# Performance work log

Measured on AMD Instinct MI355X. Metric: run time of the kernel, lower is better.

## Reference

```python
import jax, jax.numpy as jnp
import numpy as np

H = 2048   # hidden_size
NH = 32    # n_head
HS = 64    # head_size
B, T = 2, 4096
D_DECAY, D_AAA, D_MV, D_GATE = 96, 96, 64, 256


def setup_inputs() -> dict:
    key = jax.random.key(0)
    ks = jax.random.split(key, 30)
    rn = lambda k, s, sc=0.02: jax.random.normal(k, s, jnp.float32) * sc
    d = {}
    d['x'] = jax.random.normal(ks[0], (B, T, H), jnp.float32)
    d['shift_state_in'] = jax.random.normal(ks[1], (B, H), jnp.float32)
    d['wkv_state_in'] = jnp.zeros((B, NH, HS, HS), jnp.float32)
    d['v_first_val'] = jax.random.normal(ks[2], (B, T, H), jnp.float32)
    for i, n in enumerate(['x_r', 'x_w', 'x_k', 'x_v', 'x_a', 'x_g']):
        d[n] = jax.random.uniform(ks[3 + i], (H,), jnp.float32)
    d['w0'] = rn(ks[9], (H,)) - 4.0
    d['w1'] = rn(ks[10], (H, D_DECAY)); d['w2'] = rn(ks[11], (D_DECAY, H))
    d['a0'] = rn(ks[12], (H,)); d['a1'] = rn(ks[13], (H, D_AAA)); d['a2'] = rn(ks[14], (D_AAA, H))
    d['v0'] = rn(ks[15], (H,)) + 1.0; d['v1'] = rn(ks[16], (H, D_MV)); d['v2'] = rn(ks[17], (D_MV, H))
    d['g1'] = rn(ks[18], (H, D_GATE)); d['g2'] = rn(ks[19], (D_GATE, H))
    d['k_k'] = jnp.full((H,), 0.85, jnp.float32)
    d['k_a'] = jnp.ones((H,), jnp.float32)
    d['r_k'] = rn(ks[20], (NH, HS))
    s = 1.0 / np.sqrt(H)
    d['W_r'] = jax.random.normal(ks[21], (H, H), jnp.float32) * s
    d['W_k'] = jax.random.normal(ks[22], (H, H), jnp.float32) * s
    d['W_v'] = jax.random.normal(ks[23], (H, H), jnp.float32) * s
    d['W_o'] = jax.random.normal(ks[24], (H, H), jnp.float32) * s
    d['ln_w'] = jnp.ones((H,), jnp.float32)
    d['ln_b'] = jnp.zeros((H,), jnp.float32)
    return d


def _forward(x, shift_state_in, wkv_state_in, v_first_val, x_r, x_w, x_k, x_v, x_a, x_g,
             w0, w1, w2, a0, a1, a2, v0, v1, v2, g1, g2, k_k, k_a, r_k,
             W_r, W_k, W_v, W_o, ln_w, ln_b):
    Bx, Tx, C = x.shape
    # token shift: previous token embedding (shift_state for t=0)
    xprev = jnp.concatenate([shift_state_in[:, None, :], x[:, :-1]], axis=1)
    dx = xprev - x
    xr, xw, xk, xv, xa, xg = (x + dx * m for m in (x_r, x_w, x_k, x_v, x_a, x_g))
    r = xr @ W_r.T
    k = xk @ W_k.T
    v = xv @ W_v.T
    # soft-clamped log-decay (<= -0.5)
    w_raw = -jax.nn.softplus(-(w0 + jnp.tanh(xw @ w1) @ w2)) - 0.5
    # layer_id > 0: residual mix with first-layer value
    v = v + (v_first_val - v) * jax.nn.sigmoid(v0 + (xv @ v1) @ v2)
    a = jax.nn.sigmoid(a0 + (xa @ a1) @ a2)          # in-context learning rate
    g = jax.nn.sigmoid(xg @ g1) @ g2                 # output gate
    kk = (k * k_k).reshape(Bx, Tx, NH, HS)
    kk = kk / jnp.maximum(jnp.linalg.norm(kk, axis=-1, keepdims=True), 1e-12)  # F.normalize
    kk = kk.reshape(Bx, Tx, C)
    k = k * (1.0 + (a - 1.0) * k_a)
    w = jnp.exp(-jnp.exp(w_raw))                     # per-channel decay in (0,1)
    heads = lambda t: t.reshape(Bx, Tx, NH, HS).transpose(1, 0, 2, 3)  # [T,B,NH,HS]
    rs, ws, ks_, vs, kks, as_ = map(heads, (r, w, k, v, kk, a))

    def step(S, inp):
        # S: [B,NH,HS(value),HS(key)]
        rt, wt, kt, vt, kkt, at = inp
        sa = jnp.einsum('bhvk,bhk->bhv', S, -kkt)
        S = (S * wt[:, :, None, :]
             + sa[:, :, :, None] * (kkt * at)[:, :, None, :]
             + vt[:, :, :, None] * kt[:, :, None, :])
        return S, jnp.einsum('bhvk,bhk->bhv', S, rt)

    wkv_state_out, y = jax.lax.scan(step, wkv_state_in, (rs, ws, ks_, vs, kks, as_))
    y = y.transpose(1, 0, 2, 3)                      # [B,T,NH,HS]
    # GroupNorm(n_head groups, eps=1e-5*head_size)
    mu = y.mean(-1, keepdims=True)
    var = y.var(-1, keepdims=True)
    y = ((y - mu) / jnp.sqrt(var + 1e-5 * HS)).reshape(Bx, Tx, C) * ln_w + ln_b
    rk = (r.reshape(Bx, Tx, NH, HS) * k.reshape(Bx, Tx, NH, HS) * r_k).sum(-1, keepdims=True)
    y = y + (rk * v.reshape(Bx, Tx, NH, HS)).reshape(Bx, Tx, C)
    out = (y * g) @ W_o.T
    return out, x[:, -1], wkv_state_out, v_first_val


def reference(x, shift_state_in, wkv_state_in, v_first_val, x_r, x_w, x_k, x_v, x_a, x_g,
              w0, w1, w2, a0, a1, a2, v0, v1, v2, g1, g2, k_k, k_a, r_k,
              W_r, W_k, W_v, W_o, ln_w, ln_b):
    return _forward(x, shift_state_in, wkv_state_in, v_first_val, x_r, x_w, x_k, x_v, x_a, x_g,
                    w0, w1, w2, a0, a1, a2, v0, v1, v2, g1, g2, k_k, k_a, r_k,
                    W_r, W_k, W_v, W_o, ln_w, ln_b)
```

## Files before the change

### kernel.cpp

```cpp
#include <hip/hip_runtime.h>

typedef unsigned short u16;
typedef __attribute__((ext_vector_type(4))) float f32x4;
typedef __attribute__((ext_vector_type(8))) __bf16 bf16x8;
typedef __attribute__((ext_vector_type(8))) unsigned short u16x8;
typedef __attribute__((ext_vector_type(4))) unsigned short u16x4;

#define DI static __device__ __forceinline__

DI float bfu2f(u16 u){ unsigned int x = ((unsigned int)u)<<16; float f; __builtin_memcpy(&f,&x,4); return f; }
DI u16 f2bfu(float f){ __bf16 h = (__bf16)f; u16 u; __builtin_memcpy(&u,&h,2); return u; }
DI float sigm(float x){ return 1.f/(1.f+expf(-x)); }

DI void gload_lds16(const void* g, void* l) {
  __builtin_amdgcn_global_load_lds(
      (const __attribute__((address_space(1))) unsigned int*)g,
      (__attribute__((address_space(3))) unsigned int*)l, 16, 0, 0);
}

template<bool OBF16>
__global__ __launch_bounds__(256) void gemm128_k(
    const u16* __restrict__ A, const u16* __restrict__ Bt,
    void* __restrict__ Cp, int M, int N, int K)
{
  __shared__ alignas(16) u16 As[128*64];
  __shared__ alignas(16) u16 Bs[128*64];
  const int tid = threadIdx.x;
  const int wid = tid >> 6, lane = tid & 63;
  const int wm = wid >> 1, wn = wid & 1;
  const int l15 = lane & 15, q = lane >> 4;
  const int m0 = blockIdx.x * 128, n0 = blockIdx.y * 128;
  const int sr = (wid << 3) + (lane >> 3);
  const int sc = (lane & 7) << 3;
  f32x4 acc[4][4];
  #pragma unroll
  for (int i=0;i<4;i++)
    #pragma unroll
    for (int j=0;j<4;j++) acc[i][j] = f32x4{0.f,0.f,0.f,0.f};

  char* la = (char*)As + (size_t)wid*1024;
  char* lb = (char*)Bs + (size_t)wid*1024;
  for (int k0 = 0; k0 < K; k0 += 64) {
    const u16* ga = A  + (size_t)(m0 + sr)*K + k0 + sc;
    const u16* gb = Bt + (size_t)(n0 + sr)*K + k0 + sc;
    #pragma unroll
    for (int it = 0; it < 4; ++it) {
      gload_lds16(ga + (size_t)(32*it)*K, la + it*4096);
      gload_lds16(gb + (size_t)(32*it)*K, lb + it*4096);
    }
    __syncthreads();
    #pragma unroll
    for (int ks = 0; ks < 64; ks += 32) {
      bf16x8 af[4], bfv[4];
      #pragma unroll
      for (int i=0;i<4;i++) af[i]  = *(const bf16x8*)&As[(wm*64 + i*16 + l15)*64 + ks + q*8];
      #pragma unroll
      for (int j=0;j<4;j++) bfv[j] = *(const bf16x8*)&Bs[(wn*64 + j*16 + l15)*64 + ks + q*8];
      #pragma unroll
      for (int i=0;i<4;i++)
        #pragma unroll
        for (int j=0;j<4;j++)
          acc[i][j] = __builtin_amdgcn_mfma_f32_16x16x32_bf16(af[i], bfv[j], acc[i][j], 0, 0, 0);
    }
    __syncthreads();
  }
  #pragma unroll
  for (int i=0;i<4;i++)
    #pragma unroll
    for (int j=0;j<4;j++)
      #pragma unroll
      for (int rr=0;rr<4;rr++) {
        const int gm = m0 + wm*64 + i*16 + q*4 + rr;
        const int gn = n0 + wn*64 + j*16 + l15;
        const size_t o = (size_t)gm * (size_t)N + gn;
        if constexpr (OBF16) ((u16*)Cp)[o] = f2bfu(acc[i][j][rr]);
        else                 ((float*)Cp)[o] = acc[i][j][rr];
      }
}

constexpr int LDW = 72;

template<bool MIX, bool WNK, bool ABF16, bool OBF16, int EPI=0>
__global__ __launch_bounds__(256) void gemm_k(
    const void* __restrict__ Ap, const float* __restrict__ dxp, const float* __restrict__ mixp,
    const float* __restrict__ Wp, void* __restrict__ Cp, int M, int N, int K)
{
  __shared__ alignas(16) __bf16 As[64*LDW];
  __shared__ alignas(16) __bf16 Bs[64*LDW];
  const int tid = threadIdx.x;
  const int m0 = blockIdx.x * 64;
  const int n0 = blockIdx.y * 64;
  const int lane = tid & 63, wid = tid >> 6;
  const int wm = wid >> 1, wn = wid & 1;
  const int l15 = lane & 15, q = lane >> 4;
  f32x4 acc[2][2] = {{{0.f,0.f,0.f,0.f},{0.f,0.f,0.f,0.f}},
                     {{0.f,0.f,0.f,0.f},{0.f,0.f,0.f,0.f}}};

  for (int k0 = 0; k0 < K; k0 += 64) {
    {
      const int kc = (tid & 7) * 8;
      const int r0 = tid >> 3;
      #pragma unroll
      for (int it = 0; it < 2; ++it) {
        const int row = r0 + 32*it;
        const size_t gmK = (size_t)(m0 + row) * (size_t)K;
        const int gk = k0 + kc;
        if constexpr (ABF16) {
          const u16* A16 = (const u16*)Ap;
          u16x8 u;
          if (gk + 7 < K) u = *(const u16x8*)(A16 + gmK + gk);
          else {
            #pragma unroll
            for (int e=0;e<8;e++) u[e] = (gk+e < K) ? A16[gmK + gk + e] : (u16)0;
          }
          *(u16x8*)&As[row*LDW + kc] = u;
        } else {
          const float* A32 = (const float*)Ap;
          float f[8];
          if (gk + 7 < K) {
            f32x4 va = *(const f32x4*)(A32 + gmK + gk);
            f32x4 vb = *(const f32x4*)(A32 + gmK + gk + 4);
            if constexpr (MIX) {
              f32x4 d0 = *(const f32x4*)(dxp + gmK + gk);
              f32x4 d1 = *(const f32x4*)(dxp + gmK + gk + 4);
              f32x4 c0 = *(const f32x4*)(mixp + gk);
              f32x4 c1 = *(const f32x4*)(mixp + gk + 4);
              va = va + d0*c0; vb = vb + d1*c1;
            }
            #pragma unroll
            for (int e=0;e<4;e++){ f[e]=va[e]; f[4+e]=vb[e]; }
          } else {
            #pragma unroll
            for (int e=0;e<8;e++){
              const int kk2 = gk+e;
              float xv = 0.f;
              if (kk2 < K) {
                xv = A32[gmK + kk2];
                if constexpr (MIX) xv = fmaf(dxp[gmK+kk2], mixp[kk2], xv);
              }
              f[e] = xv;
            }
          }
          bf16x8 v8;
          #pragma unroll
          for (int e=0;e<8;e++) v8[e] = (__bf16)f[e];
          *(bf16x8*)&As[row*LDW + kc] = v8;
        }
      }
    }
    if constexpr (WNK) {
      const int kc = (tid & 7) * 8;
      const int r0 = tid >> 3;
      #pragma unroll
      for (int it = 0; it < 2; ++it) {
        const int row = r0 + 32*it;
        const int gn = n0 + row;
        const int gk = k0 + kc;
        float f[8];
        if (gn < N && gk + 7 < K) {
          const size_t o = (size_t)gn * (size_t)K + gk;
          f32x4 va = *(const f32x4*)(Wp + o);
          f32x4 vb = *(const f32x4*)(Wp + o + 4);
          #pragma unroll
          for (int e=0;e<4;e++){ f[e]=va[e]; f[4+e]=vb[e]; }
        } else {
          #pragma unroll
          for (int e=0;e<8;e++) f[e] = (gn < N && gk+e < K) ? Wp[(size_t)gn*K + gk + e] : 0.f;
        }
        bf16x8 v8;
        #pragma unroll
        for (int e=0;e<8;e++) v8[e] = (__bf16)f[e];
        *(bf16x8*)&Bs[row*LDW + kc] = v8;
      }
    } else {
      const int nc = (tid & 15) * 4;
      const int kr = tid >> 4;
      #pragma unroll
      for (int it = 0; it < 4; ++it) {
        const int kk = kr + 16*it;
        const int gk = k0 + kk;
        f32x4 v = {0.f,0.f,0.f,0.f};
        if (gk < K) {
          const int gn = n0 + nc;
          if (gn + 3 < N) v = *(const f32x4*)(Wp + (size_t)gk*N + gn);
          else {
            #pragma unroll
            for (int e=0;e<4;e++) if (gn+e < N) v[e] = Wp[(size_t)gk*N + gn + e];
          }
        }
        #pragma unroll
        for (int e=0;e<4;e++) Bs[(nc+e)*LDW + kk] = (__bf16)v[e];
      }
    }
    __syncthreads();
    #pragma unroll
    for (int ks = 0; ks < 64; ks += 32) {
      bf16x8 af[2], bfv[2];
      #pragma unroll
      for (int i=0;i<2;i++) af[i]  = *(const bf16x8*)&As[(wm*32 + i*16 + l15)*LDW + ks + q*8];
      #pragma unroll
      for (int i=0;i<2;i++) bfv[i] = *(const bf16x8*)&Bs[(wn*32 + i*16 + l15)*LDW + ks + q*8];
      #pragma unroll
      for (int i=0;i<2;i++)
        #pragma unroll
        for (int j=0;j<2;j++)
          acc[i][j] = __builtin_amdgcn_mfma_f32_16x16x32_bf16(af[i], bfv[j], acc[i][j], 0, 0, 0);
    }
    __syncthreads();
  }
  #pragma unroll
  for (int i=0;i<2;i++) {
    #pragma unroll
    for (int j=0;j<2;j++) {
      #pragma unroll
      for (int rr=0;rr<4;rr++) {
        const int gm = m0 + wm*32 + i*16 + q*4 + rr;
        const int gn = n0 + wn*32 + j*16 + l15;
        if (gn < N) {
          const size_t o = (size_t)gm * (size_t)N + gn;
          if constexpr (EPI == 1) {
            float* C = (float*)Cp;
            const float s = sigm(mixp[gn] + acc[i][j][rr]);
            const float vG = C[o];
            C[o] = vG + (dxp[o] - vG) * s;
          } else if constexpr (OBF16) {
            ((u16*)Cp)[o] = f2bfu(acc[i][j][rr]);
          } else {
            ((float*)Cp)[o] = acc[i][j][rr];
          }
        }
      }
    }
  }
}

__global__ void mix_cast_k(const float* __restrict__ x, const float* __restrict__ shift,
    const float* __restrict__ mr, const float* __restrict__ mw, const float* __restrict__ mk,
    const float* __restrict__ mv, const float* __restrict__ ma, const float* __restrict__ mg,
    u16* __restrict__ xr_b, u16* __restrict__ xw_b, u16* __restrict__ xk_b,
    u16* __restrict__ xv_b, u16* __restrict__ xa_b, u16* __restrict__ xg_b,
    float* __restrict__ xlast, int T_, int B_)
{
  const int Hh = 2048;
  size_t e4 = (size_t)blockIdx.x*blockDim.x + threadIdx.x;
  size_t total4 = (size_t)B_*T_*Hh/4;
  if (e4 >= total4) return;
  size_t e = e4*4;
  size_t th = (size_t)T_*Hh;
  size_t b = e / th; size_t rem = e - b*th;
  int t = (int)(rem / Hh); int c = (int)(rem & (Hh-1));
  f32x4 xv4 = *(const f32x4*)(x+e);
  f32x4 xp = t ? *(const f32x4*)(x+e-Hh) : *(const f32x4*)(shift + b*Hh + c);
  f32x4 dx = xp - xv4;
  if (t == T_-1) *(f32x4*)(xlast + b*Hh + c) = xv4;
  #define EMIT(mp, dst) { \
    f32x4 mc = *(const f32x4*)(mp + c); \
    f32x4 r_ = xv4 + dx*mc; \
    u16x4 o_; \
    o_[0]=f2bfu(r_[0]); o_[1]=f2bfu(r_[1]); o_[2]=f2bfu(r_[2]); o_[3]=f2bfu(r_[3]); \
    *(u16x4*)(dst + e) = o_; }
  EMIT(mr, xr_b) EMIT(mw, xw_b) EMIT(mk, xk_b)
  EMIT(mv, xv_b) EMIT(ma, xa_b) EMIT(mg, xg_b)
  #undef EMIT
}

__global__ void castw_k(const float* __restrict__ src, u16* __restrict__ dst, long n4){
  long i = (long)blockIdx.x*blockDim.x + threadIdx.x;
  if (i < n4) {
    f32x4 v = ((const f32x4*)src)[i];
    u16x4 o; o[0]=f2bfu(v[0]); o[1]=f2bfu(v[1]); o[2]=f2bfu(v[2]); o[3]=f2bfu(v[3]);
    ((u16x4*)dst)[i] = o;
  }
}

__global__ void ew_tanh_k(u16* p, long n){
  long i = (long)blockIdx.x*blockDim.x + threadIdx.x;
  if (i < n) p[i] = f2bfu(tanhf(bfu2f(p[i])));
}
__global__ void ew_sig_k(u16* p, long n){
  long i = (long)blockIdx.x*blockDim.x + threadIdx.x;
  if (i < n) p[i] = f2bfu(sigm(bfu2f(p[i])));
}
__global__ void ew_w_k(float* p, const float* __restrict__ w0, long n){
  long i = (long)blockIdx.x*blockDim.x + threadIdx.x;
  if (i < n) {
    int c = (int)(i & 2047);
    float z = -(w0[c] + p[i]);
    float sp = (z > 20.f) ? z : log1pf(expf(z));
    p[i] = expf(-expf(-sp - 0.5f));
  }
}
__global__ void ew_a_k(u16* p, const float* __restrict__ a0, long n){
  long i = (long)blockIdx.x*blockDim.x + threadIdx.x;
  if (i < n) { int c = (int)(i & 2047); p[i] = f2bfu(sigm(a0[c] + bfu2f(p[i]))); }
}
__global__ void copy4_k(float* __restrict__ dst, const float* __restrict__ src, long n4){
  long i = (long)blockIdx.x*blockDim.x + threadIdx.x;
  if (i < n4) ((f32x4*)dst)[i] = ((const f32x4*)src)[i];
}

__global__ __launch_bounds__(64) __attribute__((amdgpu_waves_per_eu(1, 4)))
void scan_k(
    const u16* __restrict__ rb, const float* __restrict__ wb, const u16* __restrict__ kb,
    const float* __restrict__ vb, const u16* __restrict__ ab,
    const float* __restrict__ kkw, const float* __restrict__ kaw,
    const float* __restrict__ S0, float* __restrict__ yb, float* __restrict__ Sout, int T_)
{
  const int Hh = 2048, NHl = 32;
  const int blk = blockIdx.x;
  const int b = blk >> 5, h = blk & 31;
  const int lane = threadIdx.x;
  float S[64];
  const size_t sbase = (((size_t)b*NHl + h)*64 + lane)*64;
  #pragma unroll
  for (int i=0;i<64;i++) S[i] = S0[sbase+i];
  const float kkc = kkw[h*64+lane], kac = kaw[h*64+lane];
  __shared__ alignas(16) float lw[64], lkk[64], lka[64], lke[64], lr[64];
  size_t idx = (size_t)b*T_*Hh + (size_t)h*64 + lane;
  float rv = bfu2f(rb[idx]), wv = wb[idx], kv = bfu2f(kb[idx]), vv = vb[idx], av = bfu2f(ab[idx]);
  for (int t=0; t<T_; ++t) {
    float kk = kv * kkc;
    float ssum = kk*kk;
    #pragma unroll
    for (int m=1;m<64;m<<=1) ssum += __shfl_xor(ssum, m, 64);
    float inv = 1.f / fmaxf(sqrtf(ssum), 1e-12f);
    float kkn = kk * inv;
    float ke  = kv * (1.f + (av - 1.f)*kac);
    lw[lane]=wv; lkk[lane]=kkn; lka[lane]=kkn*av; lke[lane]=ke; lr[lane]=rv;
    const float vt = vv;
    __syncthreads();
    float nrv=0.f,nwv=0.f,nkv=0.f,nvv=0.f,nav=0.f;
    if (t+1 < T_) {
      const size_t ni = idx + Hh;
      nrv = bfu2f(rb[ni]); nwv = wb[ni]; nkv = bfu2f(kb[ni]); nvv = vb[ni]; nav = bfu2f(ab[ni]);
    }
    const f32x4* KK4 = (const f32x4*)lkk;
    const f32x4* W4  = (const f32x4*)lw;
    const f32x4* KA4 = (const f32x4*)lka;
    const f32x4* KE4 = (const f32x4*)lke;
    const f32x4* R4  = (const f32x4*)lr;
    float sa0=0.f,sa1=0.f,sa2=0.f,sa3=0.f;
    #pragma unroll
    for (int qq=0;qq<16;qq++){
      f32x4 k4 = KK4[qq];
      sa0 = fmaf(S[4*qq+0], k4[0], sa0);
      sa1 = fmaf(S[4*qq+1], k4[1], sa1);
      sa2 = fmaf(S[4*qq+2], k4[2], sa2);
      sa3 = fmaf(S[4*qq+3], k4[3], sa3);
    }
    const float sa = -((sa0+sa1)+(sa2+sa3));
    float y0=0.f,y1=0.f,y2=0.f,y3=0.f;
    #pragma unroll
    for (int qq=0;qq<16;qq++){
      f32x4 w4=W4[qq], a4=KA4[qq], e4=KE4[qq], r4=R4[qq];
      float s_;
      s_ = fmaf(vt, e4[0], fmaf(sa, a4[0], S[4*qq+0]*w4[0])); S[4*qq+0]=s_; y0 = fmaf(s_, r4[0], y0);
      s_ = fmaf(vt, e4[1], fmaf(sa, a4[1], S[4*qq+1]*w4[1])); S[4*qq+1]=s_; y1 = fmaf(s_, r4[1], y1);
      s_ = fmaf(vt, e4[2], fmaf(sa, a4[2], S[4*qq+2]*w4[2])); S[4*qq+2]=s_; y2 = fmaf(s_, r4[2], y2);
      s_ = fmaf(vt, e4[3], fmaf(sa, a4[3], S[4*qq+3]*w4[3])); S[4*qq+3]=s_; y3 = fmaf(s_, r4[3], y3);
    }
    yb[idx] = (y0+y1)+(y2+y3);
    __syncthreads();
    rv=nrv; wv=nwv; kv=nkv; vv=nvv; av=nav;
    idx += Hh;
  }
  #pragma unroll
  for (int i=0;i<64;i++) Sout[sbase+i] = S[i];
}

__global__ __launch_bounds__(128) __attribute__((amdgpu_waves_per_eu(1, 4)))
void chunk_mu_k(
    const float* __restrict__ wb, const u16* __restrict__ kb,
    const float* __restrict__ vb, const u16* __restrict__ ab,
    const float* __restrict__ kkw, const float* __restrict__ kaw,
    float* __restrict__ Mbuf, float* __restrict__ Ubuf, int T_, int NC)
{
  const int Hh = 2048;
  const int ch = blockIdx.x;
  const int c  = ch % NC;
  const int bh = ch / NC;
  const int b = bh >> 5, h = bh & 31;
  const int lane = threadIdx.x & 63;
  const int wvv  = threadIdx.x >> 6;

  float S[64];
  const bool idrow = (wvv == 0);
  #pragma unroll
  for (int i=0;i<64;i++) S[i] = (idrow && lane == i) ? 1.f : 0.f;

  const int hc = h*64 + lane;
  const float kkc = kkw[hc], kac = kaw[hc];

  __shared__ alignas(16) float LA[2][4][64];
  float* Lw  = LA[wvv][0];
  float* Lkk = LA[wvv][1];
  float* Lka = LA[wvv][2];
  float* Lke = LA[wvv][3];

  size_t idx = ((size_t)b*T_ + (size_t)c*64)*Hh + h*64 + lane;
  float kv = bfu2f(kb[idx]), wv_ = wb[idx], av = bfu2f(ab[idx]), vv = vb[idx];

  for (int j=0; j<64; ++j) {
    float kk = kv * kkc;
    float ssum = kk*kk;
    #pragma unroll
    for (int m=1;m<64;m<<=1) ssum += __shfl_xor(ssum, m, 64);
    float inv = 1.f / fmaxf(sqrtf(ssum), 1e-12f);
    float kkn = kk * inv;
    Lw[lane]=wv_; Lkk[lane]=kkn; Lka[lane]=kkn*av; Lke[lane]=kv*(1.f+(av-1.f)*kac);
    const float vtv = vv;
    __syncthreads();
    float nk=0.f,nw=0.f,na=0.f,nv=0.f;
    if (j+1 < 64) {
      const size_t ni = idx + Hh;
      nk = bfu2f(kb[ni]); nw = wb[ni]; na = bfu2f(ab[ni]); nv = vb[ni];
    }
    const f32x4* KK4 = (const f32x4*)Lkk;
    const f32x4* W4  = (const f32x4*)Lw;
    const f32x4* KA4 = (const f32x4*)Lka;
    const f32x4* KE4 = (const f32x4*)Lke;
    float sa0=0.f,sa1=0.f,sa2=0.f,sa3=0.f;
    #pragma unroll
    for (int qq=0;qq<16;qq++){
      f32x4 k4 = KK4[qq];
      sa0 = fmaf(S[4*qq+0], k4[0], sa0);
      sa1 = fmaf(S[4*qq+1], k4[1], sa1);
      sa2 = fmaf(S[4*qq+2], k4[2], sa2);
      sa3 = fmaf(S[4*qq+3], k4[3], sa3);
    }
    const float sa = -((sa0+sa1)+(sa2+sa3));
    if (idrow) {
      #pragma unroll
      for (int qq=0;qq<16;qq++){
        f32x4 w4=W4[qq], a4=KA4[qq];
        S[4*qq+0] = fmaf(sa, a4[0], S[4*qq+0]*w4[0]);
        S[4*qq+1] = fmaf(sa, a4[1], S[4*qq+1]*w4[1]);
        S[4*qq+2] = fmaf(sa, a4[2], S[4*qq+2]*w4[2]);
        S[4*qq+3] = fmaf(sa, a4[3], S[4*qq+3]*w4[3]);
      }
    } else {
      #pragma unroll
      for (int qq=0;qq<16;qq++){
        f32x4 w4=W4[qq], a4=KA4[qq], e4=KE4[qq];
        S[4*qq+0] = fmaf(vtv, e4[0], fmaf(sa, a4[0], S[4*qq+0]*w4[0]));
        S[4*qq+1] = fmaf(vtv, e4[1], fmaf(sa, a4[1], S[4*qq+1]*w4[1]));
        S[4*qq+2] = fmaf(vtv, e4[2], fmaf(sa, a4[2], S[4*qq+2]*w4[2]));
        S[4*qq+3] = fmaf(vtv, e4[3], fmaf(sa, a4[3], S[4*qq+3]*w4[3]));
      }
    }
    __syncthreads();
    kv=nk; wv_=nw; av=na; vv=nv;
    idx += Hh;
  }
  float* dst = (idrow ? Mbuf : Ubuf) + (size_t)ch*4096 + (size_t)lane*64;
  #pragma unroll
  for (int qq=0;qq<16;qq++)
    *(f32x4*)(dst + 4*qq) = f32x4{S[4*qq+0],S[4*qq+1],S[4*qq+2],S[4*qq+3]};
}

__global__ __launch_bounds__(256) void propagate_k(
    const float* __restrict__ Mbuf, const float* __restrict__ Ubuf,
    const float* __restrict__ S0, float* __restrict__ SSbuf, float* __restrict__ Sout, int NC)
{
  const int bh   = blockIdx.x >> 2;
  const int v0r  = (blockIdx.x & 3) * 16;
  const int tid  = threadIdx.x;
  const int lane = tid & 63;
  const int wvv  = tid >> 6;

  __shared__ float MT[64*65];
  __shared__ float Srow[16][64];

  #pragma unroll
  for (int i=0;i<4;i++) {
    const int v = v0r + wvv*4 + i;
    Srow[wvv*4+i][lane] = S0[((size_t)bh*64 + v)*64 + lane];
  }

  const size_t mbase = (size_t)bh * NC * 4096;
  f32x4 mreg[4];
  #pragma unroll
  for (int it=0; it<4; ++it)
    mreg[it] = *(const f32x4*)(Mbuf + mbase + it*1024 + tid*4);

  for (int c=0; c<NC; ++c) {
    const size_t chB = mbase + (size_t)c*4096;
    #pragma unroll
    for (int it=0; it<4; ++it) {
      const int base = it*1024 + tid*4;
      const int j = base >> 6;
      const int k = base & 63;
      #pragma unroll
      for (int e=0;e<4;e++) MT[(k+e)*65 + j] = mreg[it][e];
    }
    __syncthreads();
    if (c+1 < NC) {
      #pragma unroll
      for (int it=0; it<4; ++it)
        mreg[it] = *(const f32x4*)(Mbuf + chB + 4096 + it*1024 + tid*4);
    }
    #pragma unroll
    for (int i=0;i<4;i++)
      SSbuf[chB + (size_t)(v0r + wvv*4 + i)*64 + lane] = Srow[wvv*4+i][lane];
    float u[4];
    #pragma unroll
    for (int i=0;i<4;i++)
      u[i] = Ubuf[chB + (size_t)(v0r + wvv*4 + i)*64 + lane];
    float acc[4] = {0.f,0.f,0.f,0.f};
    #pragma unroll
    for (int j4=0; j4<16; ++j4) {
      float m0_ = MT[lane*65 + j4*4 + 0];
      float m1_ = MT[lane*65 + j4*4 + 1];
      float m2_ = MT[lane*65 + j4*4 + 2];
      float m3_ = MT[lane*65 + j4*4 + 3];
      #pragma unroll
      for (int i=0;i<4;i++) {
        f32x4 s4 = *(const f32x4*)&Srow[wvv*4+i][j4*4];
        acc[i] = fmaf(s4[0], m0_, acc[i]);
        acc[i] = fmaf(s4[1], m1_, acc[i]);
        acc[i] = fmaf(s4[2], m2_, acc[i]);
        acc[i] = fmaf(s4[3], m3_, acc[i]);
      }
    }
    #pragma unroll
    for (int i=0;i<4;i++) Srow[wvv*4+i][lane] = acc[i] + u[i];
    __syncthreads();
  }
  #pragma unroll
  for (int i=0;i<4;i++) {
    const int v = v0r + wvv*4 + i;
    Sout[((size_t)bh*64 + v)*64 + lane] = Srow[wvv*4+i][lane];
  }
}

__global__ __launch_bounds__(64) __attribute__((amdgpu_waves_per_eu(1, 4)))
void replay_k(
    const u16* __restrict__ rb, const float* __restrict__ wb, const u16* __restrict__ kb,
    const float* __restrict__ vb, const u16* __restrict__ ab,
    const float* __restrict__ kkw, const float* __restrict__ kaw,
    const float* __restrict__ SSbuf, float* __restrict__ yb, int T_, int NC)
{
  const int Hh = 2048;
  const int ch = blockIdx.x;
  const int c  = ch % NC;
  const int bh = ch / NC;
  const int b = bh >> 5, h = bh & 31;
  const int lane = threadIdx.x;
  float S[64];
  const float* sp = SSbuf + (size_t)ch*4096 + (size_t)lane*64;
  #pragma unroll
  for (int qq=0;qq<16;qq++){
    f32x4 v4 = *(const f32x4*)(sp + 4*qq);
    S[4*qq+0]=v4[0]; S[4*qq+1]=v4[1]; S[4*qq+2]=v4[2]; S[4*qq+3]=v4[3];
  }
  const float kkc = kkw[h*64+lane], kac = kaw[h*64+lane];
  __shared__ alignas(16) float lw[64], lkk[64], lka[64], lke[64], lr[64];
  size_t idx = ((size_t)b*T_ + (size_t)c*64)*Hh + (size_t)h*64 + lane;
  float rv = bfu2f(rb[idx]), wv = wb[idx], kv = bfu2f(kb[idx]), vv = vb[idx], av = bfu2f(ab[idx]);
  for (int t=0; t<64; ++t) {
    float kk = kv * kkc;
    float ssum = kk*kk;
    #pragma unroll
    for (int m=1;m<64;m<<=1) ssum += __shfl_xor(ssum, m, 64);
    float inv = 1.f / fmaxf(sqrtf(ssum), 1e-12f);
    float kkn = kk * inv;
    float ke  = kv * (1.f + (av - 1.f)*kac);
    lw[lane]=wv; lkk[lane]=kkn; lka[lane]=kkn*av; lke[lane]=ke; lr[lane]=rv;
    const float vt = vv;
    __syncthreads();
    float nrv=0.f,nwv=0.f,nkv=0.f,nvv=0.f,nav=0.f;
    if (t+1 < 64) {
      const size_t ni = idx + Hh;
      nrv = bfu2f(rb[ni]); nwv = wb[ni]; nkv = bfu2f(kb[ni]); nvv = vb[ni]; nav = bfu2f(ab[ni]);
    }
    const f32x4* KK4 = (const f32x4*)lkk;
    const f32x4* W4  = (const f32x4*)lw;
    const f32x4* KA4 = (const f32x4*)lka;
    const f32x4* KE4 = (const f32x4*)lke;
    const f32x4* R4  = (const f32x4*)lr;
    float sa0=0.f,sa1=0.f,sa2=0.f,sa3=0.f;
    #pragma unroll
    for (int qq=0;qq<16;qq++){
      f32x4 k4 = KK4[qq];
      sa0 = fmaf(S[4*qq+0], k4[0], sa0);
      sa1 = fmaf(S[4*qq+1], k4[1], sa1);
      sa2 = fmaf(S[4*qq+2], k4[2], sa2);
      sa3 = fmaf(S[4*qq+3], k4[3], sa3);
    }
    const float sa = -((sa0+sa1)+(sa2+sa3));
    float y0=0.f,y1=0.f,y2=0.f,y3=0.f;
    #pragma unroll
    for (int qq=0;qq<16;qq++){
      f32x4 w4=W4[qq], a4=KA4[qq], e4=KE4[qq], r4=R4[qq];
      float s_;
      s_ = fmaf(vt, e4[0], fmaf(sa, a4[0], S[4*qq+0]*w4[0])); S[4*qq+0]=s_; y0 = fmaf(s_, r4[0], y0);
      s_ = fmaf(vt, e4[1], fmaf(sa, a4[1], S[4*qq+1]*w4[1])); S[4*qq+1]=s_; y1 = fmaf(s_, r4[1], y1);
      s_ = fmaf(vt, e4[2], fmaf(sa, a4[2], S[4*qq+2]*w4[2])); S[4*qq+2]=s_; y2 = fmaf(s_, r4[2], y2);
      s_ = fmaf(vt, e4[3], fmaf(sa, a4[3], S[4*qq+3]*w4[3])); S[4*qq+3]=s_; y3 = fmaf(s_, r4[3], y3);
    }
    yb[idx] = (y0+y1)+(y2+y3);
    __syncthreads();
    rv=nrv; wv=nwv; kv=nkv; vv=nvv; av=nav;
    idx += Hh;
  }
}

__global__ __launch_bounds__(256) void post_k(
    const float* __restrict__ yb, const u16* __restrict__ rb, const u16* __restrict__ kb,
    const u16* __restrict__ ab, const u16* __restrict__ gb, const float* __restrict__ vb,
    const float* __restrict__ kaw, const float* __restrict__ rkw,
    const float* __restrict__ lnw, const float* __restrict__ lnb, u16* __restrict__ zb)
{
  const int wid = threadIdx.x >> 6, lane = threadIdx.x & 63;
  const size_t unit = (size_t)blockIdx.x*4 + wid;
  const size_t bt = unit >> 5; const int h = (int)(unit & 31);
  const size_t idx = bt*2048 + (size_t)h*64 + lane;
  const int hc = h*64 + lane;
  const float yv = yb[idx];
  const float rv = bfu2f(rb[idx]), kv = bfu2f(kb[idx]), av = bfu2f(ab[idx]);
  const float ke = kv*(1.f + (av-1.f)*kaw[hc]);
  float s1 = yv, s2 = yv*yv, rk = rv*ke*rkw[hc];
  #pragma unroll
  for (int m=1;m<64;m<<=1){
    s1 += __shfl_xor(s1,m,64);
    s2 += __shfl_xor(s2,m,64);
    rk += __shfl_xor(rk,m,64);
  }
  const float mean = s1 * (1.f/64.f);
  const float var  = s2 * (1.f/64.f) - mean*mean;
  const float rstd = rsqrtf(var + 6.4e-4f);
  const float zn = (yv-mean)*rstd*lnw[hc] + lnb[hc] + rk*vb[idx];
  zb[idx] = f2bfu(zn * bfu2f(gb[idx]));
}

extern "C" void kernel_launch(void* const* d_in, const int* in_sizes, int n_in,
                              void* d_out, int out_size, void* d_ws, size_t ws_size,
                              hipStream_t stream)
{
  const float* x      = (const float*)d_in[0];
  const float* shift  = (const float*)d_in[1];
  const float* wkv0   = (const float*)d_in[2];
  const float* vfirst = (const float*)d_in[3];
  const float* xr = (const float*)d_in[4];
  const float* xw = (const float*)d_in[5];
  const float* xk = (const float*)d_in[6];
  const float* xv = (const float*)d_in[7];
  const float* xa = (const float*)d_in[8];
  const float* xg = (const float*)d_in[9];
  const float* w0 = (const float*)d_in[10];
  const float* w1 = (const float*)d_in[11];
  const float* w2 = (const float*)d_in[12];
  const float* a0 = (const float*)d_in[13];
  const float* a1 = (const float*)d_in[14];
  const float* a2 = (const float*)d_in[15];
  const float* v0 = (const float*)d_in[16];
  const float* v1 = (const float*)d_in[17];
  const float* v2 = (const float*)d_in[18];
  const float* g1 = (const float*)d_in[19];
  const float* g2 = (const float*)d_in[20];
  const float* k_k = (const float*)d_in[21];
  const float* k_a = (const float*)d_in[22];
  const float* r_k = (const float*)d_in[23];
  const float* W_r = (const float*)d_in[24];
  const float* W_k = (const float*)d_in[25];
  const float* W_v = (const float*)d_in[26];
  const float* W_o = (const float*)d_in[27];
  const float* ln_w = (const float*)d_in[28];
  const float* ln_b = (const float*)d_in[29];

  const int H = 2048, NH = 32;
  const int BH = in_sizes[1];
  const int B  = BH / H;
  const long BTH = (long)in_sizes[0];
  const int T  = (int)(BTH / BH);
  const int M  = (int)(BTH / H);

  float* out0 = (float*)d_out;
  float* out1 = out0 + BTH;
  float* out2 = out1 + BH;
  float* out3 = out2 + (size_t)B*NH*64*64;

  char* ws = (char*)d_ws;
  u16* mixb = (u16*)ws;  ws += (size_t)BTH*12;
  u16* xr_b = mixb + 0*BTH;
  u16* xw_b = mixb + 1*BTH;
  u16* xk_b = mixb + 2*BTH;
  u16* xv_b = mixb + 3*BTH;
  u16* xa_b = mixb + 4*BTH;
  u16* xg_b = mixb + 5*BTH;
  float* Mbuf  = (float*)mixb;
  float* Ubuf  = Mbuf + BTH;
  float* SSbuf = Ubuf + BTH;
  u16*   zb16  = (u16*)mixb;
  u16* rb   = (u16*)ws;  ws += BTH*2;
  u16* kb   = (u16*)ws;  ws += BTH*2;
  u16* ab   = (u16*)ws;  ws += BTH*2;
  u16* gb   = (u16*)ws;  ws += BTH*2;
  u16* wr16 = (u16*)ws;  ws += (size_t)H*H*2;
  u16* wk16 = (u16*)ws;  ws += (size_t)H*H*2;
  u16* wv16 = (u16*)ws;  ws += (size_t)H*H*2;
  u16* wo16 = (u16*)ws;  ws += (size_t)H*H*2;
  u16* h1w  = (u16*)ws;  ws += (size_t)M*96*2;
  u16* h1a  = (u16*)ws;  ws += (size_t)M*96*2;
  u16* h1v  = (u16*)ws;  ws += (size_t)M*64*2;
  u16* h1g  = (u16*)ws;  ws += (size_t)M*256*2;
  float* dxz = (float*)ws; ws += BTH*4;
  const size_t ws_need = (size_t)(ws - (char*)d_ws);
  const bool chunked = (ws_size >= ws_need) && (T % 64 == 0);
  const bool big_ok  = (M % 128 == 0);
  (void)n_in; (void)out_size;

  const dim3 blk(256);
  auto gg  = [&](int N){ return dim3(M/64, (N+63)/64); };
  auto gg128 = [&](int N){ return dim3(M/128, N/128); };

  mix_cast_k<<<dim3((unsigned)((BTH/4 + 255)/256)), blk, 0, stream>>>(
      x, shift, xr, xw, xk, xv, xa, xg, xr_b, xw_b, xk_b, xv_b, xa_b, xg_b, out1, T, B);

  {
    const long n4 = (long)H*H/4;
    const dim3 gw((unsigned)((n4 + 255)/256));
    castw_k<<<gw, blk, 0, stream>>>(W_r, wr16, n4);
    castw_k<<<gw, blk, 0, stream>>>(W_k, wk16, n4);
    castw_k<<<gw, blk, 0, stream>>>(W_v, wv16, n4);
    castw_k<<<gw, blk, 0, stream>>>(W_o, wo16, n4);
  }

  gemm_k<false,false,true,true><<<gg(96),  blk, 0, stream>>>(xw_b, nullptr, nullptr, w1, h1w, M, 96,  H);
  gemm_k<false,false,true,true><<<gg(96),  blk, 0, stream>>>(xa_b, nullptr, nullptr, a1, h1a, M, 96,  H);
  gemm_k<false,false,true,true><<<gg(64),  blk, 0, stream>>>(xv_b, nullptr, nullptr, v1, h1v, M, 64,  H);
  gemm_k<false,false,true,true><<<gg(256), blk, 0, stream>>>(xg_b, nullptr, nullptr, g1, h1g, M, 256, H);

  ew_tanh_k<<<dim3((unsigned)(((long)M*96 + 255)/256)),  blk, 0, stream>>>(h1w, (long)M*96);
  ew_sig_k <<<dim3((unsigned)(((long)M*256 + 255)/256)), blk, 0, stream>>>(h1g, (long)M*256);

  if (big_ok) {
    gemm128_k<true ><<<gg128(H), blk, 0, stream>>>(xr_b, wr16, rb,   M, H, H);
    gemm128_k<true ><<<gg128(H), blk, 0, stream>>>(xk_b, wk16, kb,   M, H, H);
    gemm128_k<false><<<gg128(H), blk, 0, stream>>>(xv_b, wv16, out3, M, H, H);
  } else {
    gemm_k<false,true,true,true ><<<gg(H), blk, 0, stream>>>(xr_b, nullptr, nullptr, W_r, rb,   M, H, H);
    gemm_k<false,true,true,true ><<<gg(H), blk, 0, stream>>>(xk_b, nullptr, nullptr, W_k, kb,   M, H, H);
    gemm_k<false,true,true,false><<<gg(H), blk, 0, stream>>>(xv_b, nullptr, nullptr, W_v, out3, M, H, H);
  }

  gemm_k<false,false,true,false  ><<<gg(H), blk, 0, stream>>>(h1w, nullptr, nullptr, w2, dxz, M, H, 96);
  gemm_k<false,false,true,true   ><<<gg(H), blk, 0, stream>>>(h1a, nullptr, nullptr, a2, ab,  M, H, 96);
  gemm_k<false,false,true,false,1><<<gg(H), blk, 0, stream>>>(h1v, vfirst,  v0,      v2, out3, M, H, 64);
  gemm_k<false,false,true,true   ><<<gg(H), blk, 0, stream>>>(h1g, nullptr, nullptr, g2, gb,  M, H, 256);

  const unsigned nbB = (unsigned)((BTH + 255)/256);
  ew_w_k<<<dim3(nbB), blk, 0, stream>>>(dxz, w0, BTH);
  ew_a_k<<<dim3(nbB), blk, 0, stream>>>(ab, a0, BTH);

  if (chunked) {
    const int NC = T / 64;
    const int CH = B * NH * NC;
    chunk_mu_k <<<dim3(CH),     dim3(128), 0, stream>>>(dxz, kb, out3, ab, k_k, k_a, Mbuf, Ubuf, T, NC);
    propagate_k<<<dim3(B*NH*4), blk,       0, stream>>>(Mbuf, Ubuf, wkv0, SSbuf, out2, NC);
    replay_k   <<<dim3(CH),     dim3(64),  0, stream>>>(rb, dxz, kb, out3, ab, k_k, k_a, SSbuf, out0, T, NC);
  } else {
    scan_k<<<dim3(B*NH), dim3(64), 0, stream>>>(rb, dxz, kb, out3, ab, k_k, k_a, wkv0, out0, out2, T);
  }

  post_k<<<dim3((unsigned)((size_t)M*NH/4)), blk, 0, stream>>>(out0, rb, kb, ab, gb, out3,
                                                               k_a, r_k, ln_w, ln_b, zb16);

  copy4_k<<<dim3((unsigned)((BTH/4 + 255)/256)), blk, 0, stream>>>(out3, vfirst, BTH/4);

  if (big_ok) {
    gemm128_k<false><<<gg128(H), blk, 0, stream>>>(zb16, wo16, out0, M, H, H);
  } else {
    gemm_k<false,true,true,false><<<gg(H), blk, 0, stream>>>(zb16, nullptr, nullptr, W_o, out0, M, H, H);
  }
}
```

Baseline: 2.053 ms.

## Precompute kk inverse norms, double-buffer LDS, split chunk_mu into single-wave blocks

A new kernel precomputes the inverse squared norm of kk for each token and head. This removes the 64-lane shuffle reduction and sqrt from the serial recurrence in chunk_mu_k and replay_k, which now apply the norm as a scalar multiply on sa. Both kernels double-buffer their LDS inputs so the next step's values are written before a single barrier per step, instead of two. chunk_mu_k is split into two 64-thread blocks per chunk (identity part and value part), which doubles the grid. The r2 buffer reuses the h1w workspace after its last consumer; the math is reassociated slightly, so rounding can differ from before.

```diff
diff --git a/kernel.cpp b/kernel.cpp
--- a/kernel.cpp
+++ b/kernel.cpp
@@ -299,6 +299,26 @@
   if (i < n4) ((f32x4*)dst)[i] = ((const f32x4*)src)[i];
 }
 
+__global__ __launch_bounds__(256) void rnorm_k(
+    const u16* __restrict__ kb, const float* __restrict__ kkw, float* __restrict__ r2)
+{
+  const size_t bt = blockIdx.x;
+  const int tid = threadIdx.x;
+  const int c0 = tid << 3;
+  u16x8 kv8 = *(const u16x8*)(kb + bt*2048 + c0);
+  f32x4 ka_ = *(const f32x4*)(kkw + c0);
+  f32x4 kb_ = *(const f32x4*)(kkw + c0 + 4);
+  float s = 0.f;
+  #pragma unroll
+  for (int e=0;e<4;e++){ float kk = bfu2f(kv8[e])*ka_[e];   s = fmaf(kk,kk,s); }
+  #pragma unroll
+  for (int e=0;e<4;e++){ float kk = bfu2f(kv8[4+e])*kb_[e]; s = fmaf(kk,kk,s); }
+  s += __shfl_xor(s, 1, 64);
+  s += __shfl_xor(s, 2, 64);
+  s += __shfl_xor(s, 4, 64);
+  if ((tid & 7) == 0) r2[bt*32 + (tid>>3)] = 1.f/fmaxf(s, 1e-24f);
+}
+
 __global__ __launch_bounds__(64) __attribute__((amdgpu_waves_per_eu(1, 4)))
 void scan_k(
     const u16* __restrict__ rb, const float* __restrict__ wb, const u16* __restrict__ kb,
@@ -368,57 +388,59 @@
   for (int i=0;i<64;i++) Sout[sbase+i] = S[i];
 }
 
-__global__ __launch_bounds__(128) __attribute__((amdgpu_waves_per_eu(1, 4)))
-void chunk_mu_k(
+__global__ __launch_bounds__(64) void chunk_mu_k(
     const float* __restrict__ wb, const u16* __restrict__ kb,
     const float* __restrict__ vb, const u16* __restrict__ ab,
     const float* __restrict__ kkw, const float* __restrict__ kaw,
+    const float* __restrict__ r2b,
     float* __restrict__ Mbuf, float* __restrict__ Ubuf, int T_, int NC)
 {
-  const int Hh = 2048;
-  const int ch = blockIdx.x;
+  const int bid = blockIdx.x;
+  const int ch  = bid >> 1;
+  const bool idrow = ((bid & 1) == 0);
   const int c  = ch % NC;
   const int bh = ch / NC;
   const int b = bh >> 5, h = bh & 31;
-  const int lane = threadIdx.x & 63;
-  const int wvv  = threadIdx.x >> 6;
+  const int lane = threadIdx.x;
 
   float S[64];
-  const bool idrow = (wvv == 0);
   #pragma unroll
   for (int i=0;i<64;i++) S[i] = (idrow && lane == i) ? 1.f : 0.f;
 
   const int hc = h*64 + lane;
   const float kkc = kkw[hc], kac = kaw[hc];
 
-  __shared__ alignas(16) float LA[2][4][64];
-  float* Lw  = LA[wvv][0];
-  float* Lkk = LA[wvv][1];
-  float* Lka = LA[wvv][2];
-  float* Lke = LA[wvv][3];
-
-  size_t idx = ((size_t)b*T_ + (size_t)c*64)*Hh + h*64 + lane;
-  float kv = bfu2f(kb[idx]), wv_ = wb[idx], av = bfu2f(ab[idx]), vv = vb[idx];
+  __shared__ alignas(16) float LB[2][4][64];
+
+  size_t idx = ((size_t)b*T_ + (size_t)c*64)*2048 + hc;
+  size_t r2i = ((size_t)b*T_ + (size_t)c*64)*32 + h;
+
+  {
+    const float kv = bfu2f(kb[idx]);
+    const float av = bfu2f(ab[idx]);
+    const float kk = kv*kkc;
+    LB[0][0][lane] = wb[idx];
+    LB[0][1][lane] = kk;
+    LB[0][2][lane] = kk*av;
+    if (!idrow) LB[0][3][lane] = kv*(1.f+(av-1.f)*kac);
+  }
+  float vv = idrow ? 0.f : vb[idx];
+  float r2 = r2b[r2i];
+  __syncthreads();
 
   for (int j=0; j<64; ++j) {
-    float kk = kv * kkc;
-    float ssum = kk*kk;
-    #pragma unroll
-    for (int m=1;m<64;m<<=1) ssum += __shfl_xor(ssum, m, 64);
-    float inv = 1.f / fmaxf(sqrtf(ssum), 1e-12f);
-    float kkn = kk * inv;
-    Lw[lane]=wv_; Lkk[lane]=kkn; Lka[lane]=kkn*av; Lke[lane]=kv*(1.f+(av-1.f)*kac);
-    const float vtv = vv;
-    __syncthreads();
-    float nk=0.f,nw=0.f,na=0.f,nv=0.f;
+    const int cur = j & 1;
+    float nk=0.f,nw=0.f,na=0.f,nv=0.f,nr2=0.f;
     if (j+1 < 64) {
-      const size_t ni = idx + Hh;
-      nk = bfu2f(kb[ni]); nw = wb[ni]; na = bfu2f(ab[ni]); nv = vb[ni];
-    }
-    const f32x4* KK4 = (const f32x4*)Lkk;
-    const f32x4* W4  = (const f32x4*)Lw;
-    const f32x4* KA4 = (const f32x4*)Lka;
-    const f32x4* KE4 = (const f32x4*)Lke;
+      const size_t ni = idx + 2048;
+      nk = bfu2f(kb[ni]); nw = wb[ni]; na = bfu2f(ab[ni]);
+      if (!idrow) nv = vb[ni];
+      nr2 = r2b[r2i + 32];
+    }
+    const f32x4* W4  = (const f32x4*)LB[cur][0];
+    const f32x4* KK4 = (const f32x4*)LB[cur][1];
+    const f32x4* KA4 = (const f32x4*)LB[cur][2];
+    const f32x4* KE4 = (const f32x4*)LB[cur][3];
     float sa0=0.f,sa1=0.f,sa2=0.f,sa3=0.f;
     #pragma unroll
     for (int qq=0;qq<16;qq++){
@@ -428,7 +450,8 @@
       sa2 = fmaf(S[4*qq+2], k4[2], sa2);
       sa3 = fmaf(S[4*qq+3], k4[3], sa3);
     }
-    const float sa = -((sa0+sa1)+(sa2+sa3));
+    const float sa = -((sa0+sa1)+(sa2+sa3)) * r2;
+    const float vtv = vv;
     if (idrow) {
       #pragma unroll
       for (int qq=0;qq<16;qq++){
@@ -448,9 +471,16 @@
         S[4*qq+3] = fmaf(vtv, e4[3], fmaf(sa, a4[3], S[4*qq+3]*w4[3]));
       }
     }
-    __syncthreads();
-    kv=nk; wv_=nw; av=na; vv=nv;
-    idx += Hh;
+    if (j+1 < 64) {
+      const float kk = nk*kkc;
+      LB[cur^1][0][lane] = nw;
+      LB[cur^1][1][lane] = kk;
+      LB[cur^1][2][lane] = kk*na;
+      if (!idrow) LB[cur^1][3][lane] = nk*(1.f+(na-1.f)*kac);
+    }
+    __syncthreads();
+    vv = nv; r2 = nr2;
+    idx += 2048; r2i += 32;
   }
   float* dst = (idrow ? Mbuf : Ubuf) + (size_t)ch*4096 + (size_t)lane*64;
   #pragma unroll
@@ -533,14 +563,13 @@
   }
 }
 
-__global__ __launch_bounds__(64) __attribute__((amdgpu_waves_per_eu(1, 4)))
-void replay_k(
+__global__ __launch_bounds__(64) void replay_k(
     const u16* __restrict__ rb, const float* __restrict__ wb, const u16* __restrict__ kb,
     const float* __restrict__ vb, const u16* __restrict__ ab,
     const float* __restrict__ kkw, const float* __restrict__ kaw,
+    const float* __restrict__ r2b,
     const float* __restrict__ SSbuf, float* __restrict__ yb, int T_, int NC)
 {
-  const int Hh = 2048;
   const int ch = blockIdx.x;
   const int c  = ch % NC;
   const int bh = ch / NC;
@@ -553,31 +582,38 @@
     f32x4 v4 = *(const f32x4*)(sp + 4*qq);
     S[4*qq+0]=v4[0]; S[4*qq+1]=v4[1]; S[4*qq+2]=v4[2]; S[4*qq+3]=v4[3];
   }
-  const float kkc = kkw[h*64+lane], kac = kaw[h*64+lane];
-  __shared__ alignas(16) float lw[64], lkk[64], lka[64], lke[64], lr[64];
-  size_t idx = ((size_t)b*T_ + (size_t)c*64)*Hh + (size_t)h*64 + lane;
-  float rv = bfu2f(rb[idx]), wv = wb[idx], kv = bfu2f(kb[idx]), vv = vb[idx], av = bfu2f(ab[idx]);
+  const int hc = h*64 + lane;
+  const float kkc = kkw[hc], kac = kaw[hc];
+  __shared__ alignas(16) float LB[2][5][64];
+  size_t idx = ((size_t)b*T_ + (size_t)c*64)*2048 + hc;
+  size_t r2i = ((size_t)b*T_ + (size_t)c*64)*32 + h;
+  {
+    const float kv = bfu2f(kb[idx]);
+    const float av = bfu2f(ab[idx]);
+    const float kk = kv*kkc;
+    LB[0][0][lane] = wb[idx];
+    LB[0][1][lane] = kk;
+    LB[0][2][lane] = kk*av;
+    LB[0][3][lane] = kv*(1.f+(av-1.f)*kac);
+    LB[0][4][lane] = bfu2f(rb[idx]);
+  }
+  float vv = vb[idx];
+  float r2 = r2b[r2i];
+  __syncthreads();
+
   for (int t=0; t<64; ++t) {
-    float kk = kv * kkc;
-    float ssum = kk*kk;
-    #pragma unroll
-    for (int m=1;m<64;m<<=1) ssum += __shfl_xor(ssum, m, 64);
-    float inv = 1.f / fmaxf(sqrtf(ssum), 1e-12f);
-    float kkn = kk * inv;
-    float ke  = kv * (1.f + (av - 1.f)*kac);
-    lw[lane]=wv; lkk[lane]=kkn; lka[lane]=kkn*av; lke[lane]=ke; lr[lane]=rv;
-    const float vt = vv;
-    __syncthreads();
-    float nrv=0.f,nwv=0.f,nkv=0.f,nvv=0.f,nav=0.f;
+    const int cur = t & 1;
+    float nr=0.f,nw=0.f,nk=0.f,nv=0.f,na=0.f,nr2=0.f;
     if (t+1 < 64) {
-      const size_t ni = idx + Hh;
-      nrv = bfu2f(rb[ni]); nwv = wb[ni]; nkv = bfu2f(kb[ni]); nvv = vb[ni]; nav = bfu2f(ab[ni]);
-    }
-    const f32x4* KK4 = (const f32x4*)lkk;
-    const f32x4* W4  = (const f32x4*)lw;
-    const f32x4* KA4 = (const f32x4*)lka;
-    const f32x4* KE4 = (const f32x4*)lke;
-    const f32x4* R4  = (const f32x4*)lr;
+      const size_t ni = idx + 2048;
+      nr = bfu2f(rb[ni]); nw = wb[ni]; nk = bfu2f(kb[ni]); nv = vb[ni]; na = bfu2f(ab[ni]);
+      nr2 = r2b[r2i + 32];
+    }
+    const f32x4* W4  = (const f32x4*)LB[cur][0];
+    const f32x4* KK4 = (const f32x4*)LB[cur][1];
+    const f32x4* KA4 = (const f32x4*)LB[cur][2];
+    const f32x4* KE4 = (const f32x4*)LB[cur][3];
+    const f32x4* R4  = (const f32x4*)LB[cur][4];
     float sa0=0.f,sa1=0.f,sa2=0.f,sa3=0.f;
     #pragma unroll
     for (int qq=0;qq<16;qq++){
@@ -587,7 +623,8 @@
       sa2 = fmaf(S[4*qq+2], k4[2], sa2);
       sa3 = fmaf(S[4*qq+3], k4[3], sa3);
     }
-    const float sa = -((sa0+sa1)+(sa2+sa3));
+    const float sa = -((sa0+sa1)+(sa2+sa3)) * r2;
+    const float vt = vv;
     float y0=0.f,y1=0.f,y2=0.f,y3=0.f;
     #pragma unroll
     for (int qq=0;qq<16;qq++){
@@ -599,9 +636,17 @@
       s_ = fmaf(vt, e4[3], fmaf(sa, a4[3], S[4*qq+3]*w4[3])); S[4*qq+3]=s_; y3 = fmaf(s_, r4[3], y3);
     }
     yb[idx] = (y0+y1)+(y2+y3);
-    __syncthreads();
-    rv=nrv; wv=nwv; kv=nkv; vv=nvv; av=nav;
-    idx += Hh;
+    if (t+1 < 64) {
+      const float kk = nk*kkc;
+      LB[cur^1][0][lane] = nw;
+      LB[cur^1][1][lane] = kk;
+      LB[cur^1][2][lane] = kk*na;
+      LB[cur^1][3][lane] = nk*(1.f+(na-1.f)*kac);
+      LB[cur^1][4][lane] = nr;
+    }
+    __syncthreads();
+    vv = nv; r2 = nr2;
+    idx += 2048; r2i += 32;
   }
 }
 
@@ -705,6 +750,7 @@
   u16* h1v  = (u16*)ws;  ws += (size_t)M*64*2;
   u16* h1g  = (u16*)ws;  ws += (size_t)M*256*2;
   float* dxz = (float*)ws; ws += BTH*4;
+  float* r2b = (float*)h1w;
   const size_t ws_need = (size_t)(ws - (char*)d_ws);
   const bool chunked = (ws_size >= ws_need) && (T % 64 == 0);
   const bool big_ok  = (M % 128 == 0);
@@ -745,6 +791,7 @@
   }
 
   gemm_k<false,false,true,false  ><<<gg(H), blk, 0, stream>>>(h1w, nullptr, nullptr, w2, dxz, M, H, 96);
+  rnorm_k<<<dim3((unsigned)M), blk, 0, stream>>>(kb, k_k, r2b);
   gemm_k<false,false,true,true   ><<<gg(H), blk, 0, stream>>>(h1a, nullptr, nullptr, a2, ab,  M, H, 96);
   gemm_k<false,false,true,false,1><<<gg(H), blk, 0, stream>>>(h1v, vfirst,  v0,      v2, out3, M, H, 64);
   gemm_k<false,false,true,true   ><<<gg(H), blk, 0, stream>>>(h1g, nullptr, nullptr, g2, gb,  M, H, 256);
@@ -756,9 +803,9 @@
   if (chunked) {
     const int NC = T / 64;
     const int CH = B * NH * NC;
-    chunk_mu_k <<<dim3(CH),     dim3(128), 0, stream>>>(dxz, kb, out3, ab, k_k, k_a, Mbuf, Ubuf, T, NC);
+    chunk_mu_k <<<dim3(2*CH),   dim3(64),  0, stream>>>(dxz, kb, out3, ab, k_k, k_a, r2b, Mbuf, Ubuf, T, NC);
     propagate_k<<<dim3(B*NH*4), blk,       0, stream>>>(Mbuf, Ubuf, wkv0, SSbuf, out2, NC);
-    replay_k   <<<dim3(CH),     dim3(64),  0, stream>>>(rb, dxz, kb, out3, ab, k_k, k_a, SSbuf, out0, T, NC);
+    replay_k   <<<dim3(CH),     dim3(64),  0, stream>>>(rb, dxz, kb, out3, ab, k_k, k_a, r2b, SSbuf, out0, T, NC);
   } else {
     scan_k<<<dim3(B*NH), dim3(64), 0, stream>>>(rb, dxz, kb, out3, ab, k_k, k_a, wkv0, out0, out2, T);
   }
```

Measured after the change: 1.989 ms. 1.03x faster.
